# Optimization experiments

Measured on AMD Instinct MI355X. Metric: run time of the kernel, lower is better.

## Reference

```python
import jax, jax.numpy as jnp
import numpy as np

N, K, CIN, COUT = 1_000_000, 27, 32, 64
EPS = 1e-5


def setup_inputs() -> dict:
    key = jax.random.key(0)
    ks = jax.random.split(key, 8)
    feats = jax.random.normal(ks[0], (N, CIN), dtype=jnp.float32)
    nbr_idx = jax.random.randint(ks[1], (N, K), 0, N, dtype=jnp.int32)
    mask = jax.random.bernoulli(ks[2], 0.7, (N, K))
    # center offset (self) is always present in a submanifold conv
    mask = mask.at[:, K // 2].set(True)
    nbr_idx = nbr_idx.at[:, K // 2].set(jnp.arange(N, dtype=jnp.int32))
    w_scale1 = 1.0 / np.sqrt(K * CIN)
    w_scale2 = 1.0 / np.sqrt(K * COUT)
    W1 = jax.random.normal(ks[3], (K, CIN, COUT), dtype=jnp.float32) * w_scale1
    W2 = jax.random.normal(ks[4], (K, COUT, COUT), dtype=jnp.float32) * w_scale2
    gamma1 = jnp.ones((COUT,), jnp.float32)
    beta1 = jnp.zeros((COUT,), jnp.float32)
    gamma2 = jnp.ones((COUT,), jnp.float32)
    beta2 = jnp.zeros((COUT,), jnp.float32)
    return {"feats": feats, "W1": W1, "W2": W2, "gamma1": gamma1,
            "beta1": beta1, "gamma2": gamma2, "beta2": beta2,
            "nbr_idx": nbr_idx, "mask": mask}


def _submanifold_conv(feats, W, nbr_idx, maskf):
    """Gather-GEMM-accumulate over K kernel offsets.

    feats: [N, Cin]; W: [K, Cin, Cout]; nbr_idx: [N, K]; maskf: [N, K] float.
    Scans over the small fixed K axis to avoid a [N, K, Cin] intermediate.
    """
    n = feats.shape[0]
    cout = W.shape[2]

    def body(acc, xs):
        Wk, idx_k, m_k = xs  # [Cin,Cout], [N], [N]
        g = feats[idx_k] * m_k[:, None]  # gather + mask: [N, Cin]
        return acc + g @ Wk, None

    init = jnp.zeros((n, cout), feats.dtype)
    out, _ = jax.lax.scan(body, init, (W, nbr_idx.T, maskf.T))
    return out


def _bn_relu(x, gamma, beta):
    # training-mode batch norm over active sites
    mu = jnp.mean(x, axis=0)
    var = jnp.var(x, axis=0)
    y = (x - mu) * jax.lax.rsqrt(var + EPS) * gamma + beta
    return jax.nn.relu(y)


def reference(feats, W1, W2, gamma1, beta1, gamma2, beta2, nbr_idx, mask):
    maskf = mask.astype(feats.dtype)
    h = _submanifold_conv(feats, W1, nbr_idx, maskf)
    h = _bn_relu(h, gamma1, beta1)
    h = _submanifold_conv(h, W2, nbr_idx, maskf)
    h = _bn_relu(h, gamma2, beta2)
    return h
```

## Files before the change

kernel.cpp:

```cpp
#include <hip/hip_runtime.h>

#define NPTS 1000000
#define KNBR 27
#define NCH 64
#define EPSV 1e-5f

typedef __attribute__((ext_vector_type(8))) short bf16x8;
typedef __attribute__((ext_vector_type(4))) float f32x4;
typedef __attribute__((ext_vector_type(8))) unsigned short ushort8;

__device__ inline unsigned short f2bf(float f) {
    unsigned int x = __float_as_uint(f);
    unsigned int r = x + 0x7FFFu + ((x >> 16) & 1u);
    return (unsigned short)(r >> 16);
}
__device__ inline float bf2f(unsigned short u) {
    return __uint_as_float(((unsigned int)u) << 16);
}

__global__ void detect_mask_kernel(const unsigned int* __restrict__ mask32,
                                   int* __restrict__ flag)
{
    __shared__ int cnt;
    if (threadIdx.x == 0) cnt = 0;
    __syncthreads();
    int c = 0;
    for (int i = threadIdx.x; i < 4096; i += 256)
        if (mask32[i] <= 1u) c++;
    atomicAdd(&cnt, c);
    __syncthreads();
    if (threadIdx.x == 0) *flag = (cnt >= 3900) ? 1 : 0;
}

__global__ __launch_bounds__(256)
void cvt_feats_kernel(const float* __restrict__ in, unsigned short* __restrict__ outp)
{
    const long nchunk = (long)NPTS * 32 / 8;
    const long stride = (long)gridDim.x * 256;
    const float4* f4 = (const float4*)in;
    ushort8* o8 = (ushort8*)outp;
    for (long i = (long)blockIdx.x * 256 + threadIdx.x; i < nchunk; i += stride) {
        float4 a = f4[2 * i], b = f4[2 * i + 1];
        ushort8 o;
        o[0] = f2bf(a.x); o[1] = f2bf(a.y); o[2] = f2bf(a.z); o[3] = f2bf(a.w);
        o[4] = f2bf(b.x); o[5] = f2bf(b.y); o[6] = f2bf(b.z); o[7] = f2bf(b.w);
        o8[i] = o;
    }
}

template<int CIN>
__global__ __launch_bounds__(256)
void transpose_w_frag_kernel(const float* __restrict__ W, unsigned short* __restrict__ wtf)
{
    const int k = blockIdx.x;
    constexpr int TOT = CIN * 64;
    for (int e = threadIdx.x; e < TOT; e += 256) {
        const int j = e & 7, l = (e >> 3) & 63, c = (e >> 9) & 3, ks = e >> 11;
        const int ci = ks * 32 + (l >> 4) * 8 + j;
        const int co = c * 16 + (l & 15);
        wtf[(size_t)k * TOT + e] = f2bf(W[((size_t)k * CIN + ci) * 64 + co]);
    }
}

template<int CIN, bool OUT_BF16>
__global__ __launch_bounds__(256, 4)
void conv_mfma_kernel(const unsigned short* __restrict__ src,
                      const unsigned short* __restrict__ wtf,
                      const int* __restrict__ nbr,
                      const unsigned char* __restrict__ mask8,
                      const int* __restrict__ mask32,
                      const int* __restrict__ mflag,
                      void* __restrict__ outp,
                      float* __restrict__ sums)
{
    constexpr int KS = CIN / 32;
    __shared__ int midx[128 * KNBR];
    __shared__ float sred[64], qred[64];

    const int t = threadIdx.x;
    const int pbase = blockIdx.x * 128;

    if (t < 64) { sred[t] = 0.f; qred[t] = 0.f; }

    const bool m32 = (*mflag != 0);
    for (int i = t; i < 128 * KNBR; i += 256) {
        const int p = i / KNBR;
        int v = -1;
        if (pbase + p < NPTS) {
            const int gi = pbase * KNBR + i;
            const bool mv = m32 ? (mask32[gi] != 0) : (mask8[gi] != 0);
            v = mv ? nbr[gi] : -1;
        }
        midx[i] = v;
    }
    __syncthreads();

    const int wave = t >> 6;
    const int lane = t & 63;
    const int lr = lane & 15;
    const int kg = lane >> 4;
    const int wpt = wave * 32;

    f32x4 acc[4][2];
#pragma unroll
    for (int c = 0; c < 4; ++c)
#pragma unroll
        for (int a = 0; a < 2; ++a) acc[c][a] = (f32x4){0.f, 0.f, 0.f, 0.f};

    const bf16x8 zero8 = {0, 0, 0, 0, 0, 0, 0, 0};
    const int mbase0 = (wpt + lr) * KNBR;

    for (int k = 0; k < KNBR; ++k) {
#pragma unroll
        for (int ks = 0; ks < KS; ++ks) {
            bf16x8 a[2];
#pragma unroll
            for (int ai = 0; ai < 2; ++ai) {
                const int mi = midx[mbase0 + ai * (16 * KNBR) + k];
                a[ai] = zero8;
                if (mi >= 0)
                    a[ai] = *(const bf16x8*)(src + (size_t)mi * CIN + ks * 32 + kg * 8);
            }
            bf16x8 b[4];
#pragma unroll
            for (int c = 0; c < 4; ++c)
                b[c] = *(const bf16x8*)(wtf + (size_t)k * (CIN * 64)
                                            + ((ks * 4 + c) * 64 + lane) * 8);
#pragma unroll
            for (int c = 0; c < 4; ++c)
#pragma unroll
                for (int ai = 0; ai < 2; ++ai)
                    acc[c][ai] = __builtin_amdgcn_mfma_f32_16x16x32_bf16(
                        a[ai], b[c], acc[c][ai], 0, 0, 0);
        }
    }

    float s[4], q[4];
#pragma unroll
    for (int c = 0; c < 4; ++c) { s[c] = 0.f; q[c] = 0.f; }

#pragma unroll
    for (int c = 0; c < 4; ++c) {
#pragma unroll
        for (int ai = 0; ai < 2; ++ai) {
#pragma unroll
            for (int r = 0; r < 4; ++r) {
                const float v = acc[c][ai][r];
                s[c] += v;
                q[c] = fmaf(v, v, q[c]);
                const int row = pbase + wpt + ai * 16 + kg * 4 + r;
                if (row < NPTS) {
                    if (OUT_BF16)
                        ((unsigned short*)outp)[(size_t)row * NCH + c * 16 + lr] = f2bf(v);
                    else
                        __builtin_nontemporal_store(
                            v, &((float*)outp)[(size_t)row * NCH + c * 16 + lr]);
                }
            }
        }
    }
#pragma unroll
    for (int c = 0; c < 4; ++c) {
        atomicAdd(&sred[c * 16 + lr], s[c]);
        atomicAdd(&qred[c * 16 + lr], q[c]);
    }
    __syncthreads();
    if (t < 64) {
        atomicAdd(&sums[t], sred[t]);
        atomicAdd(&sums[64 + t], qred[t]);
    }
}

__global__ void finalize_kernel(const float* __restrict__ sums,
                                const float* __restrict__ gamma,
                                const float* __restrict__ beta,
                                float* __restrict__ ss)
{
    const int c = threadIdx.x;
    if (c < NCH) {
        const float inv = 1.0f / (float)NPTS;
        float mu  = sums[c] * inv;
        float var = sums[NCH + c] * inv - mu * mu;
        float rs  = 1.0f / sqrtf(var + EPSV);
        float scv = gamma[c] * rs;
        ss[c]       = scv;
        ss[NCH + c] = beta[c] - mu * scv;
    }
}

__global__ __launch_bounds__(256)
void bnrelu_bf16_kernel(unsigned short* __restrict__ x, const float* __restrict__ ss)
{
    const int t = threadIdx.x;
    const int c0 = (t & 7) * 8;
    float sc[8], sh[8];
#pragma unroll
    for (int j = 0; j < 8; ++j) { sc[j] = ss[c0 + j]; sh[j] = ss[NCH + c0 + j]; }
    const long nchunk = (long)NPTS * NCH / 8;
    const long stride = (long)gridDim.x * 256;
    ushort8* x8 = (ushort8*)x;
    for (long i = (long)blockIdx.x * 256 + t; i < nchunk; i += stride) {
        ushort8 v = x8[i];
#pragma unroll
        for (int j = 0; j < 8; ++j) {
            float f = fmaxf(fmaf(bf2f(v[j]), sc[j], sh[j]), 0.0f);
            v[j] = f2bf(f);
        }
        x8[i] = v;
    }
}

__global__ __launch_bounds__(256)
void bnrelu_f32_kernel(float* __restrict__ x, const float* __restrict__ ss, long n4)
{
    const int t = threadIdx.x;
    const int c0 = (t * 4) & 63;
    const float4 sc = *(const float4*)&ss[c0];
    const float4 sh = *(const float4*)&ss[NCH + c0];
    const long stride = (long)gridDim.x * 256;
    f32x4* x4 = (f32x4*)x;
    for (long i = (long)blockIdx.x * 256 + t; i < n4; i += stride) {
        f32x4 v = __builtin_nontemporal_load(&x4[i]);
        v.x = fmaxf(fmaf(v.x, sc.x, sh.x), 0.0f);
        v.y = fmaxf(fmaf(v.y, sc.y, sh.y), 0.0f);
        v.z = fmaxf(fmaf(v.z, sc.z, sh.z), 0.0f);
        v.w = fmaxf(fmaf(v.w, sc.w, sh.w), 0.0f);
        __builtin_nontemporal_store(v, &x4[i]);
    }
}

extern "C" void kernel_launch(void* const* d_in, const int* in_sizes, int n_in,
                              void* d_out, int out_size, void* d_ws, size_t ws_size,
                              hipStream_t stream)
{
    const float* feats  = (const float*)d_in[0];
    const float* W1     = (const float*)d_in[1];
    const float* W2     = (const float*)d_in[2];
    const float* gamma1 = (const float*)d_in[3];
    const float* beta1  = (const float*)d_in[4];
    const float* gamma2 = (const float*)d_in[5];
    const float* beta2  = (const float*)d_in[6];
    const int* nbr      = (const int*)d_in[7];
    const unsigned char* mask8 = (const unsigned char*)d_in[8];
    const int* mask32          = (const int*)d_in[8];
    float* out = (float*)d_out;

    char* w = (char*)d_ws;
    unsigned short* h1  = (unsigned short*)w;
    unsigned short* fb  = (unsigned short*)(w + 128000000);
    unsigned short* wt1 = (unsigned short*)(w + 192000000);
    unsigned short* wt2 = (unsigned short*)(w + 192200704);
    float* stats        = (float*)(w + 192600000);
    int*   mflag        = (int*)(w + 192700000);

    (void)hipMemsetAsync(stats, 0, 512 * sizeof(float), stream);
    detect_mask_kernel<<<1, 256, 0, stream>>>((const unsigned int*)d_in[8], mflag);

    cvt_feats_kernel<<<2048, 256, 0, stream>>>(feats, fb);
    transpose_w_frag_kernel<32><<<KNBR, 256, 0, stream>>>(W1, wt1);
    transpose_w_frag_kernel<64><<<KNBR, 256, 0, stream>>>(W2, wt2);

    const int conv_grid = (NPTS + 127) / 128;
    const long n4 = (long)NPTS * NCH / 4;

    conv_mfma_kernel<32, true><<<conv_grid, 256, 0, stream>>>(
        fb, wt1, nbr, mask8, mask32, mflag, h1, stats);
    finalize_kernel<<<1, 64, 0, stream>>>(stats, gamma1, beta1, stats + 128);
    bnrelu_bf16_kernel<<<2048, 256, 0, stream>>>(h1, stats + 128);

    conv_mfma_kernel<64, false><<<conv_grid, 256, 0, stream>>>(
        h1, wt2, nbr, mask8, mask32, mflag, out, stats + 256);
    finalize_kernel<<<1, 64, 0, stream>>>(stats + 256, gamma2, beta2, stats + 384);
    bnrelu_f32_kernel<<<2048, 256, 0, stream>>>(out, stats + 384, n4);
}
```

Measured before the change: 1.634 ms.

## Prefetch neighbor gathers two offsets ahead with zero-row sentinel for masked entries

Masked neighbors now point at an extra all-zero sentinel row (index NPTS) in both feature buffers instead of -1. This removes the per-load branch, so gathers are unconditional. The K loop is fully unrolled with a 3-deep register ring that issues gathers two kernel offsets ahead, hiding global-load latency behind the MFMAs. Index and mask loads are marked nontemporal, occupancy is lowered to 3 waves/SIMD for the extra registers, and workspace offsets shift to make room for the sentinel rows. The risks are register pressure or spills and reduced occupancy.

```diff
diff --git a/kernel.cpp b/kernel.cpp
--- a/kernel.cpp
+++ b/kernel.cpp
@@ -48,6 +48,14 @@
     }
 }
 
+__global__ void zero_rows_kernel(unsigned short* __restrict__ fb,
+                                 unsigned short* __restrict__ h1)
+{
+    const int t = threadIdx.x;
+    if (t < 32) fb[(size_t)NPTS * 32 + t] = 0;
+    if (t < 64) h1[(size_t)NPTS * 64 + t] = 0;
+}
+
 template<int CIN>
 __global__ __launch_bounds__(256)
 void transpose_w_frag_kernel(const float* __restrict__ W, unsigned short* __restrict__ wtf)
@@ -63,7 +71,7 @@
 }
 
 template<int CIN, bool OUT_BF16>
-__global__ __launch_bounds__(256, 4)
+__global__ __launch_bounds__(256, 3)
 void conv_mfma_kernel(const unsigned short* __restrict__ src,
                       const unsigned short* __restrict__ wtf,
                       const int* __restrict__ nbr,
@@ -85,11 +93,13 @@
     const bool m32 = (*mflag != 0);
     for (int i = t; i < 128 * KNBR; i += 256) {
         const int p = i / KNBR;
-        int v = -1;
+        int v = NPTS;
         if (pbase + p < NPTS) {
             const int gi = pbase * KNBR + i;
-            const bool mv = m32 ? (mask32[gi] != 0) : (mask8[gi] != 0);
-            v = mv ? nbr[gi] : -1;
+            const int idxv = __builtin_nontemporal_load(&nbr[gi]);
+            const bool mv = m32 ? (__builtin_nontemporal_load(&mask32[gi]) != 0)
+                                : (__builtin_nontemporal_load(&mask8[gi]) != 0);
+            v = mv ? idxv : NPTS;
         }
         midx[i] = v;
     }
@@ -100,6 +110,8 @@
     const int lr = lane & 15;
     const int kg = lane >> 4;
     const int wpt = wave * 32;
+    const int mb0 = (wpt + lr) * KNBR;
+    const int mb1 = (wpt + 16 + lr) * KNBR;
 
     f32x4 acc[4][2];
 #pragma unroll
@@ -107,32 +119,55 @@
 #pragma unroll
         for (int a = 0; a < 2; ++a) acc[c][a] = (f32x4){0.f, 0.f, 0.f, 0.f};
 
-    const bf16x8 zero8 = {0, 0, 0, 0, 0, 0, 0, 0};
-    const int mbase0 = (wpt + lr) * KNBR;
-
+    const int koff = kg * 8;
+
+    bf16x8 A[3][KS][2];
+    int mi0c, mi1c;
+
+    {
+        const int a00 = midx[mb0 + 0], a01 = midx[mb1 + 0];
+        const int a10 = midx[mb0 + 1], a11 = midx[mb1 + 1];
+#pragma unroll
+        for (int ks = 0; ks < KS; ++ks) {
+            A[0][ks][0] = *(const bf16x8*)(src + (size_t)a00 * CIN + ks * 32 + koff);
+            A[0][ks][1] = *(const bf16x8*)(src + (size_t)a01 * CIN + ks * 32 + koff);
+            A[1][ks][0] = *(const bf16x8*)(src + (size_t)a10 * CIN + ks * 32 + koff);
+            A[1][ks][1] = *(const bf16x8*)(src + (size_t)a11 * CIN + ks * 32 + koff);
+        }
+        mi0c = midx[mb0 + 2];
+        mi1c = midx[mb1 + 2];
+    }
+
+#pragma unroll
     for (int k = 0; k < KNBR; ++k) {
-#pragma unroll
-        for (int ks = 0; ks < KS; ++ks) {
-            bf16x8 a[2];
-#pragma unroll
-            for (int ai = 0; ai < 2; ++ai) {
-                const int mi = midx[mbase0 + ai * (16 * KNBR) + k];
-                a[ai] = zero8;
-                if (mi >= 0)
-                    a[ai] = *(const bf16x8*)(src + (size_t)mi * CIN + ks * 32 + kg * 8);
+        if (k + 2 < KNBR) {
+#pragma unroll
+            for (int ks = 0; ks < KS; ++ks) {
+                A[(k + 2) % 3][ks][0] =
+                    *(const bf16x8*)(src + (size_t)mi0c * CIN + ks * 32 + koff);
+                A[(k + 2) % 3][ks][1] =
+                    *(const bf16x8*)(src + (size_t)mi1c * CIN + ks * 32 + koff);
             }
-            bf16x8 b[4];
+        }
+        if (k + 3 < KNBR) {
+            mi0c = midx[mb0 + k + 3];
+            mi1c = midx[mb1 + k + 3];
+        }
+        bf16x8 B[KS][4];
+#pragma unroll
+        for (int ks = 0; ks < KS; ++ks)
 #pragma unroll
             for (int c = 0; c < 4; ++c)
-                b[c] = *(const bf16x8*)(wtf + (size_t)k * (CIN * 64)
-                                            + ((ks * 4 + c) * 64 + lane) * 8);
+                B[ks][c] = *(const bf16x8*)(wtf + (size_t)k * (CIN * 64)
+                                                + ((ks * 4 + c) * 64 + lane) * 8);
+#pragma unroll
+        for (int ks = 0; ks < KS; ++ks)
 #pragma unroll
             for (int c = 0; c < 4; ++c)
 #pragma unroll
                 for (int ai = 0; ai < 2; ++ai)
                     acc[c][ai] = __builtin_amdgcn_mfma_f32_16x16x32_bf16(
-                        a[ai], b[c], acc[c][ai], 0, 0, 0);
-        }
+                        A[k % 3][ks][ai], B[ks][c], acc[c][ai], 0, 0, 0);
     }
 
     float s[4], q[4];
@@ -247,16 +282,17 @@
 
     char* w = (char*)d_ws;
     unsigned short* h1  = (unsigned short*)w;
-    unsigned short* fb  = (unsigned short*)(w + 128000000);
-    unsigned short* wt1 = (unsigned short*)(w + 192000000);
-    unsigned short* wt2 = (unsigned short*)(w + 192200704);
-    float* stats        = (float*)(w + 192600000);
-    int*   mflag        = (int*)(w + 192700000);
+    unsigned short* fb  = (unsigned short*)(w + 128000512);
+    unsigned short* wt1 = (unsigned short*)(w + 192001024);
+    unsigned short* wt2 = (unsigned short*)(w + 192112128);
+    float* stats        = (float*)(w + 192400000);
+    int*   mflag        = (int*)(w + 192500000);
 
     (void)hipMemsetAsync(stats, 0, 512 * sizeof(float), stream);
     detect_mask_kernel<<<1, 256, 0, stream>>>((const unsigned int*)d_in[8], mflag);
 
     cvt_feats_kernel<<<2048, 256, 0, stream>>>(feats, fb);
+    zero_rows_kernel<<<1, 64, 0, stream>>>(fb, h1);
     transpose_w_frag_kernel<32><<<KNBR, 256, 0, stream>>>(W1, wt1);
     transpose_w_frag_kernel<64><<<KNBR, 256, 0, stream>>>(W2, wt2);
 
```

After: 1.679 ms. 2.7% more time.
